# Performance work log

Hardware: AMD Instinct MI355X
Metric: run time of the kernel (lower is better)

Reference implementation:

```python
import jax, jax.numpy as jnp
import numpy as np

N_GRAPH = 100000
N_CAND = 1000
N_EDGES = 3200000
F_IN = 32


def _param(k, shape):
    return jax.random.normal(k, shape, dtype=jnp.float32) * 0.1


def setup_inputs() -> dict:
    key = jax.random.key(0)
    ks = jax.random.split(key, 20)
    inp = {
        "x": jax.random.normal(ks[0], (N_GRAPH, F_IN), dtype=jnp.float32),
        "candidate_set": jax.random.normal(ks[1], (N_CAND, F_IN), dtype=jnp.float32),
        "edge_index": jax.random.randint(ks[2], (2, N_EDGES), 0, N_GRAPH, dtype=jnp.int32),
        # GCN stack 32 -> 16 -> 24 -> 32
        "W1": _param(ks[3], (F_IN, 16)), "b1": jnp.zeros((16,), jnp.float32),
        "W2": _param(ks[4], (16, 24)),   "b2": jnp.zeros((24,), jnp.float32),
        "W3": _param(ks[5], (24, 32)),   "b3": jnp.zeros((32,), jnp.float32),
        # start-node MLP: 32 -> 16 -> 1
        "Ws1": _param(ks[6], (32, 16)), "bs1": jnp.zeros((16,), jnp.float32),
        "Ws2": _param(ks[7], (16, 1)),  "bs2": jnp.zeros((1,), jnp.float32),
        # end-node MLP: 32 -> 24 -> 1
        "We1": _param(ks[8], (32, 24)), "be1": jnp.zeros((24,), jnp.float32),
        "We2": _param(ks[9], (24, 1)),  "be2": jnp.zeros((1,), jnp.float32),
    }
    return inp


def _relu6(v):
    return jnp.clip(v, 0.0, 6.0)


def _gcn(h, row, col, dinv, W, b, N):
    # PyG GCNConv: h @ W, then D^-1/2 (A+I) D^-1/2 aggregation, then + bias
    h = h @ W
    norm = (dinv[row] * dinv[col])[:, None]
    return jax.ops.segment_sum(h[row] * norm, col, num_segments=N) + b


def reference(x, candidate_set, edge_index, W1, b1, W2, b2, W3, b3,
              Ws1, bs1, Ws2, bs2, We1, be1, We2, be2):
    n_graph = x.shape[0]
    h = jnp.concatenate([x, candidate_set], axis=0)  # [N, F_IN]
    N = h.shape[0]
    sl = jnp.arange(N, dtype=edge_index.dtype)
    row = jnp.concatenate([edge_index[0], sl])  # self-loops appended
    col = jnp.concatenate([edge_index[1], sl])
    deg = jax.ops.segment_sum(jnp.ones(row.shape[0], h.dtype), col, num_segments=N)
    dinv = 1.0 / jnp.sqrt(deg)  # deg >= 1 thanks to self-loops

    for W, b in ((W1, b1), (W2, b2), (W3, b3)):
        h = _gcn(h, row, col, dinv, W, b, N)  # [N, 32] at the end

    # start-node head: softmax over nodes (dim 0)
    start_probs = jax.nn.softmax(_relu6(h @ Ws1 + bs1) @ Ws2 + bs2, axis=0)  # [N,1]
    mask = jnp.ones_like(start_probs).at[n_graph:].set(0.0)  # zero out candidates
    start_probs = start_probs * mask
    start_probs = jnp.where(start_probs == 0.0, 1e-10, start_probs)
    start_probs = start_probs.squeeze()  # [N]
    start_node = jax.random.categorical(jax.random.key(42), jnp.log(start_probs))

    # end-node head
    end_probs = jax.nn.softmax(_relu6(h @ We1 + be1) @ We2 + be2, axis=0)  # [N,1]
    end_probs = end_probs.at[start_node].set(0.0)
    end_probs = jnp.where(end_probs == 0.0, 1e-10, end_probs)
    end_probs = end_probs.squeeze()  # [N]
    end_node = jax.random.categorical(jax.random.key(43), jnp.log(end_probs))

    new_edge = jnp.stack([start_node, end_node]).astype(edge_index.dtype)[:, None]
    edge_index_new = jnp.concatenate([edge_index, new_edge], axis=1)
    return (h, start_probs, end_probs, start_node, end_node, edge_index_new)
```

## Files before the change

kernel.cpp:

```cpp
#include <hip/hip_runtime.h>
#include <math.h>

#define TPB 256
#define BNODES 256
#define EPB 8192
#define SENT (-1)
#define MAXBKT 512
#define STAGE_CAP 14144

typedef _Float16 h8 __attribute__((ext_vector_type(8)));
typedef _Float16 hf;

__device__ __forceinline__ float jax_gumbel(unsigned key, unsigned i) {
  unsigned x0 = 0u, x1 = i;
  unsigned ks0 = 0u, ks1 = key, ks2 = key ^ 0x1BD11BDAu;
  x0 += ks0; x1 += ks1;
#define TFR(r) { x0 += x1; x1 = (x1 << (r)) | (x1 >> (32 - (r))); x1 ^= x0; }
  TFR(13) TFR(15) TFR(26) TFR(6)
  x0 += ks1; x1 += ks2 + 1u;
  TFR(17) TFR(29) TFR(16) TFR(24)
  x0 += ks2; x1 += ks0 + 2u;
  TFR(13) TFR(15) TFR(26) TFR(6)
  x0 += ks0; x1 += ks1 + 3u;
  TFR(17) TFR(29) TFR(16) TFR(24)
  x0 += ks1; x1 += ks2 + 4u;
  TFR(13) TFR(15) TFR(26) TFR(6)
  x0 += ks2; x1 += ks0 + 5u;
#undef TFR
  unsigned bits = x0 ^ x1;
  float f = __uint_as_float((bits >> 9) | 0x3f800000u) - 1.0f;
  float u = (f == 0.0f) ? 1.17549435e-38f : f;
  return -logf(-logf(u));
}

__global__ void hist_k(const int* __restrict__ col, int* __restrict__ hist,
                       int ne, int nbkt, int nblk) {
  __shared__ int h[1024];
  int t = threadIdx.x;
  for (int i = t; i < nbkt; i += TPB) h[i] = 0;
  __syncthreads();
  int base = blockIdx.x * EPB;
#pragma unroll
  for (int k = 0; k < EPB / TPB; k++) {
    int idx = base + k * TPB + t;
    if (idx < ne) atomicAdd(&h[col[idx] >> 8], 1);
  }
  __syncthreads();
  for (int i = t; i < nbkt; i += TPB) hist[(size_t)i * nblk + blockIdx.x] = h[i];
}

__global__ void breal_k(const int* __restrict__ hist, int* __restrict__ breal, int nblk) {
  int bkt = blockIdx.x;
  int t = threadIdx.x;
  int s = 0;
  for (int b = t; b < nblk; b += TPB) s += hist[(size_t)bkt * nblk + b];
  __shared__ int red[TPB];
  red[t] = s; __syncthreads();
  for (int st = 128; st > 0; st >>= 1) { if (t < st) red[t] += red[t + st]; __syncthreads(); }
  if (t == 0) breal[bkt] = red[0];
}

template <int PAD>
__global__ void scan1_k(const int* __restrict__ a, int* __restrict__ bsums, int n) {
  int t = threadIdx.x;
  int base = blockIdx.x * 1024 + t * 4;
  int s = 0;
#pragma unroll
  for (int k = 0; k < 4; k++) {
    int i = base + k;
    if (i < n) { int v = a[i]; if (PAD) v = (v + 15) & ~15; s += v; }
  }
  __shared__ int red[TPB];
  red[t] = s; __syncthreads();
  for (int st = 128; st > 0; st >>= 1) { if (t < st) red[t] += red[t + st]; __syncthreads(); }
  if (t == 0) bsums[blockIdx.x] = red[0];
}

__global__ void scan_single_k(int* a, int m) {
  __shared__ int sc[TPB];
  int t = threadIdx.x;
  int v[4]; int s = 0;
#pragma unroll
  for (int k = 0; k < 4; k++) { int i = t * 4 + k; v[k] = (i < m) ? a[i] : 0; s += v[k]; }
  sc[t] = s; __syncthreads();
  for (int off = 1; off < TPB; off <<= 1) {
    int add = (t >= off) ? sc[t - off] : 0;
    __syncthreads();
    sc[t] += add;
    __syncthreads();
  }
  int excl = sc[t] - s;
#pragma unroll
  for (int k = 0; k < 4; k++) { int i = t * 4 + k; if (i < m) a[i] = excl; excl += v[k]; }
  if (t == TPB - 1) a[m] = excl;
}

template <int PAD>
__global__ void scan3_k(const int* __restrict__ a, const int* __restrict__ bsums,
                        int* __restrict__ outp, int n, int nb) {
  int t = threadIdx.x;
  int base = blockIdx.x * 1024 + t * 4;
  int v[4]; int tsum = 0;
#pragma unroll
  for (int k = 0; k < 4; k++) {
    int vv = 0;
    if (base + k < n) { vv = a[base + k]; if (PAD) vv = (vv + 15) & ~15; }
    v[k] = vv; tsum += vv;
  }
  __shared__ int sc[TPB];
  sc[t] = tsum; __syncthreads();
  for (int off = 1; off < TPB; off <<= 1) {
    int add = (t >= off) ? sc[t - off] : 0;
    __syncthreads();
    sc[t] += add;
    __syncthreads();
  }
  int excl = sc[t] - tsum + bsums[blockIdx.x];
#pragma unroll
  for (int k = 0; k < 4; k++) { if (base + k < n) outp[base + k] = excl; excl += v[k]; }
  if (blockIdx.x == 0 && t == 0) outp[n] = bsums[nb];
}

__global__ void __launch_bounds__(TPB, 1)
bscatter_k(const int* __restrict__ row, const int* __restrict__ col,
           const int* __restrict__ histP, int* __restrict__ pairs,
           int ne, int nbkt, int nblk) {
  __shared__ int sbase[MAXBKT], lofs[MAXBKT], lcur[MAXBKT], lsz[MAXBKT];
  __shared__ int ssc[TPB];
  __shared__ int stage[STAGE_CAP];
  int t = threadIdx.x;
  int b = blockIdx.x;
  int i0 = 2 * t, i1 = 2 * t + 1;
  int g0 = 0, L0 = 0, g1 = 0, L1 = 0;
  if (i0 < nbkt) { size_t f = (size_t)i0 * nblk + b; g0 = histP[f]; L0 = histP[f + 1] - g0; }
  if (i1 < nbkt) { size_t f = (size_t)i1 * nblk + b; g1 = histP[f]; L1 = histP[f + 1] - g1; }
  int s = L0 + L1;
  ssc[t] = s; __syncthreads();
  for (int off = 1; off < TPB; off <<= 1) {
    int add = (t >= off) ? ssc[t - off] : 0;
    __syncthreads();
    ssc[t] += add;
    __syncthreads();
  }
  int excl = ssc[t] - s;
  if (i0 < nbkt) { sbase[i0] = g0; lofs[i0] = excl; lcur[i0] = excl; lsz[i0] = L0; }
  if (i1 < nbkt) { sbase[i1] = g1; lofs[i1] = excl + L0; lcur[i1] = excl + L0; lsz[i1] = L1; }
  __syncthreads();
  int base0 = b * EPB;
#pragma unroll
  for (int k = 0; k < EPB / TPB; k++) {
    int idx = base0 + k * TPB + t;
    if (idx < ne) {
      int c = col[idx];
      int r = row[idx];
      int p = atomicAdd(&lcur[c >> 8], 1);
      stage[p] = (r << 8) | (c & 255);
    }
  }
  __syncthreads();
  for (int i = t; i < nbkt; i += TPB) {
    int en = lcur[i], pe = lofs[i] + lsz[i];
    for (int p = en; p < pe; p++) stage[p] = SENT;
  }
  __syncthreads();
  int4* gp = (int4*)pairs;
  const int4* sp = (const int4*)stage;
  for (int i = t; i < nbkt; i += TPB) {
    int gb = sbase[i] >> 2, lb = lofs[i] >> 2, m = lsz[i] >> 2;
    for (int q = 0; q < m; q++) gp[gb + q] = sp[lb + q];
  }
}

__global__ void bbuild_k(const int* __restrict__ pairs, const int* __restrict__ histP,
                         const int* __restrict__ bbase, int nblk, int* __restrict__ rp,
                         float* __restrict__ dinv, int* __restrict__ csr, int n, int ne) {
  int bkt = blockIdx.x;
  int lo = bkt << 8;
  int t = threadIdx.x;
  int pstart = histP[(size_t)bkt * nblk];
  int pend   = histP[(size_t)(bkt + 1) * nblk];
  int rbase  = bbase[bkt];
  __shared__ int cnt[BNODES], sc[BNODES], pos[BNODES];
  cnt[t] = 0; __syncthreads();
  for (int p = pstart + t; p < pend; p += TPB) {
    int e = pairs[p];
    if (e >= 0) atomicAdd(&cnt[e & 255], 1);
  }
  __syncthreads();
  int own = cnt[t];
  sc[t] = own; __syncthreads();
  for (int off = 1; off < BNODES; off <<= 1) {
    int add = (t >= off) ? sc[t - off] : 0;
    __syncthreads();
    sc[t] += add;
    __syncthreads();
  }
  int excl = sc[t] - own;
  if (lo + t < n) {
    rp[lo + t] = rbase + excl;
    dinv[lo + t] = 1.0f / sqrtf((float)(own + 1));
  }
  pos[t] = rbase + excl;
  __syncthreads();
  for (int p = pstart + t; p < pend; p += TPB) {
    int e = pairs[p];
    if (e >= 0) {
      int q = atomicAdd(&pos[e & 255], 1);
      csr[q] = e >> 8;
    }
  }
  if (bkt == 0 && t == 0) rp[n] = ne;
}

__global__ void prep_k(const float* __restrict__ W2, const float* __restrict__ W3,
                       const float* __restrict__ b1, const float* __restrict__ b2,
                       float* __restrict__ W23, float* __restrict__ bvA, float* __restrict__ bvB) {
  int t = threadIdx.x;
  for (int idx = t; idx < 512; idx += TPB) {
    int i = idx >> 5, j = idx & 31;
    float s = 0.f;
    for (int k = 0; k < 24; k++) s += W2[i * 24 + k] * W3[k * 32 + j];
    W23[idx] = s;
  }
  __syncthreads();
  if (t < 32) {
    float sA = 0.f;
    for (int i = 0; i < 16; i++) sA += b1[i] * W23[i * 32 + t];
    bvA[t] = sA;
    float sB = 0.f;
    for (int k = 0; k < 24; k++) sB += b2[k] * W3[k * 32 + t];
    bvB[t] = sB;
  }
}

__global__ void gemm16h_k(const float* __restrict__ A, const float* __restrict__ A2, int nsplit,
                          const float* __restrict__ W, const float* __restrict__ dinv,
                          hf* __restrict__ out, int n) {
  constexpr int FIN = 32, FOUT = 16, FP = 16;
  constexpr int NODES = TPB / FP;
  __shared__ float Ws[FIN * FOUT];
  __shared__ float Hs[NODES * (FIN + 1)];
  int t = threadIdx.x;
  int base = blockIdx.x * NODES;
  for (int i = t; i < FIN * FOUT; i += TPB) Ws[i] = W[i];
  for (int i = t; i < NODES * FIN; i += TPB) {
    int nl = i / FIN, k = i - nl * FIN;
    int g = base + nl;
    float v = 0.f;
    if (g < n) v = (g < nsplit) ? A[(size_t)g * FIN + k] : A2[(size_t)(g - nsplit) * FIN + k];
    Hs[nl * (FIN + 1) + k] = v;
  }
  __syncthreads();
  int nl = t / FP, j = t % FP;
  int g = base + nl;
  if (g < n) {
    float acc = 0.f;
#pragma unroll
    for (int k = 0; k < FIN; k++) acc += Hs[nl * (FIN + 1) + k] * Ws[k * FOUT + j];
    out[(size_t)g * FOUT + j] = (hf)(acc * dinv[g]);
  }
}

__global__ void agghs_k(const h8* __restrict__ ts, const int* __restrict__ csr,
                        const int* __restrict__ rp, const float* __restrict__ dinv,
                        const float* __restrict__ sin, float* __restrict__ u_out,
                        float* __restrict__ us_out, h8* __restrict__ outv, int n) {
  int wave = blockIdx.x * (TPB / 64) + (threadIdx.x >> 6);
  int lane = threadIdx.x & 63;
  int j = lane & 1;
  int grp = (lane >> 1) & 7;
  int nl = lane >> 4;
  int c = wave * 4 + nl;
  bool valid = (c < n);
  float acc[8] = {0.f, 0.f, 0.f, 0.f, 0.f, 0.f, 0.f, 0.f};
  float accS = 0.f;
  if (valid) {
    int s = rp[c], e = rp[c + 1];
    for (int p = s + grp; p < e; p += 8) {
      int r = csr[p];
      h8 v = ts[r * 2 + j];
#pragma unroll
      for (int k = 0; k < 8; k++) acc[k] += (float)v[k];
      if (j == 0) accS += sin[r];
    }
  }
#pragma unroll
  for (int off = 2; off <= 8; off <<= 1) {
#pragma unroll
    for (int k = 0; k < 8; k++) acc[k] += __shfl_xor(acc[k], off, 64);
    accS += __shfl_xor(accS, off, 64);
  }
  if (valid && grp == 0) {
    h8 self = ts[c * 2 + j];
    float d = dinv[c];
    float scl = d * d;
    h8 o;
#pragma unroll
    for (int k = 0; k < 8; k++) o[k] = (hf)(scl * (acc[k] + (float)self[k]));
    outv[c * 2 + j] = o;
    if (j == 0) {
      float u = d * (accS + sin[c]);
      u_out[c] = u;
      if (us_out) us_out[c] = u * d;
    }
  }
}

__global__ void agghc_k(const h8* __restrict__ ts, const int* __restrict__ csr,
                        const int* __restrict__ rp, const float* __restrict__ dinv,
                        const float* __restrict__ a1, const float* __restrict__ a2,
                        const float* __restrict__ W23, const float* __restrict__ bvA,
                        const float* __restrict__ bvB, const float* __restrict__ b3,
                        float* __restrict__ out, int n) {
  __shared__ float Ws[512], vA[32], vB[32], vb[32];
  __shared__ float t3s[16][17];
  int t = threadIdx.x;
  for (int i = t; i < 512; i += TPB) Ws[i] = W23[i];
  if (t < 32) { vA[t] = bvA[t]; vB[t] = bvB[t]; vb[t] = b3[t]; }
  int wave = t >> 6;
  int lane = t & 63;
  int j = lane & 1;
  int grp = (lane >> 1) & 7;
  int nl = lane >> 4;
  int nlb = wave * 4 + nl;
  int c = blockIdx.x * 16 + nlb;
  bool valid = (c < n);
  float acc[8] = {0.f, 0.f, 0.f, 0.f, 0.f, 0.f, 0.f, 0.f};
  if (valid) {
    int s = rp[c], e = rp[c + 1];
    for (int p = s + grp; p < e; p += 8) {
      int r = csr[p];
      h8 v = ts[r * 2 + j];
#pragma unroll
      for (int k = 0; k < 8; k++) acc[k] += (float)v[k];
    }
  }
#pragma unroll
  for (int off = 2; off <= 8; off <<= 1) {
#pragma unroll
    for (int k = 0; k < 8; k++) acc[k] += __shfl_xor(acc[k], off, 64);
  }
  if (valid && grp == 0) {
    h8 self = ts[c * 2 + j];
    float d = dinv[c];
#pragma unroll
    for (int k = 0; k < 8; k++) t3s[nlb][j * 8 + k] = d * (acc[k] + (float)self[k]);
  }
  __syncthreads();
  int n2 = t >> 4, j2 = t & 15;
  int g = blockIdx.x * 16 + n2;
  if (g < n) {
    float accA = 0.f, accB = 0.f;
#pragma unroll
    for (int k = 0; k < 16; k++) {
      float h = t3s[n2][k];
      accA += h * Ws[k * 32 + j2];
      accB += h * Ws[k * 32 + j2 + 16];
    }
    float av = a1[g], bv = a2[g];
    out[(size_t)g * 32 + j2]      = accA + bv * vA[j2]      + av * vB[j2]      + vb[j2];
    out[(size_t)g * 32 + j2 + 16] = accB + bv * vA[j2 + 16] + av * vB[j2 + 16] + vb[j2 + 16];
  }
}

__global__ void heads_k(const float* __restrict__ h3,
                        const float* __restrict__ Ws1, const float* __restrict__ bs1,
                        const float* __restrict__ ws2, const float* __restrict__ bs2,
                        const float* __restrict__ We1, const float* __restrict__ be1,
                        const float* __restrict__ we2, const float* __restrict__ be2,
                        float* __restrict__ slog, float* __restrict__ elog, int n) {
  __shared__ float W1s[32 * 16], W2s[32 * 24], b1s[16], b2s[24], v1s[16], v2s[24];
  int t = threadIdx.x;
  for (int i = t; i < 32 * 16; i += TPB) W1s[i] = Ws1[i];
  for (int i = t; i < 32 * 24; i += TPB) W2s[i] = We1[i];
  if (t < 16) { b1s[t] = bs1[t]; v1s[t] = ws2[t]; }
  if (t < 24) { b2s[t] = be1[t]; v2s[t] = we2[t]; }
  __syncthreads();
  int i = blockIdx.x * TPB + t;
  if (i >= n) return;
  float row[32];
#pragma unroll
  for (int k = 0; k < 32; k++) row[k] = h3[(size_t)i * 32 + k];
  float s = bs2[0];
#pragma unroll
  for (int j = 0; j < 16; j++) {
    float a = b1s[j];
#pragma unroll
    for (int k = 0; k < 32; k++) a += row[k] * W1s[k * 16 + j];
    a = fminf(fmaxf(a, 0.f), 6.f);
    s += a * v1s[j];
  }
  float e2 = be2[0];
#pragma unroll
  for (int j = 0; j < 24; j++) {
    float a = b2s[j];
#pragma unroll
    for (int k = 0; k < 32; k++) a += row[k] * W2s[k * 24 + j];
    a = fminf(fmaxf(a, 0.f), 6.f);
    e2 += a * v2s[j];
  }
  slog[i] = s;
  elog[i] = e2;
}

__global__ void osm_k(const float* __restrict__ a, const float* __restrict__ b,
                      float* __restrict__ pm, int n) {
  int t = threadIdx.x;
  float m1 = -3.402823466e+38f, s1 = 0.f, m2 = -3.402823466e+38f, s2 = 0.f;
  for (int i = blockIdx.x * TPB + t; i < n; i += gridDim.x * TPB) {
    float x = a[i];
    if (x > m1) { s1 = s1 * expf(m1 - x) + 1.f; m1 = x; } else s1 += expf(x - m1);
    float y = b[i];
    if (y > m2) { s2 = s2 * expf(m2 - y) + 1.f; m2 = y; } else s2 += expf(y - m2);
  }
  __shared__ float sm1[TPB], ss1[TPB], sm2[TPB], ss2[TPB];
  sm1[t] = m1; ss1[t] = s1; sm2[t] = m2; ss2[t] = s2; __syncthreads();
  for (int st = 128; st > 0; st >>= 1) {
    if (t < st) {
      float M = fmaxf(sm1[t], sm1[t + st]);
      ss1[t] = ss1[t] * expf(sm1[t] - M) + ss1[t + st] * expf(sm1[t + st] - M);
      sm1[t] = M;
      float M2 = fmaxf(sm2[t], sm2[t + st]);
      ss2[t] = ss2[t] * expf(sm2[t] - M2) + ss2[t + st] * expf(sm2[t + st] - M2);
      sm2[t] = M2;
    }
    __syncthreads();
  }
  if (t == 0) {
    pm[blockIdx.x] = sm1[0]; pm[256 + blockIdx.x] = ss1[0];
    pm[512 + blockIdx.x] = sm2[0]; pm[768 + blockIdx.x] = ss2[0];
  }
}

__global__ void osm_fin_k(const float* __restrict__ pm, float* __restrict__ fsc, int nb) {
  int t = threadIdx.x;
  float m1 = (t < nb) ? pm[t] : -3.402823466e+38f;
  float s1 = (t < nb) ? pm[256 + t] : 0.f;
  float m2 = (t < nb) ? pm[512 + t] : -3.402823466e+38f;
  float s2 = (t < nb) ? pm[768 + t] : 0.f;
  __shared__ float sm1[TPB], ss1[TPB], sm2[TPB], ss2[TPB];
  sm1[t] = m1; ss1[t] = s1; sm2[t] = m2; ss2[t] = s2; __syncthreads();
  for (int st = 128; st > 0; st >>= 1) {
    if (t < st) {
      float M = fmaxf(sm1[t], sm1[t + st]);
      ss1[t] = ss1[t] * expf(sm1[t] - M) + ss1[t + st] * expf(sm1[t + st] - M);
      sm1[t] = M;
      float M2 = fmaxf(sm2[t], sm2[t + st]);
      ss2[t] = ss2[t] * expf(sm2[t] - M2) + ss2[t + st] * expf(sm2[t + st] - M2);
      sm2[t] = M2;
    }
    __syncthreads();
  }
  if (t == 0) { fsc[0] = sm1[0]; fsc[2] = ss1[0]; fsc[1] = sm2[0]; fsc[3] = ss2[0]; }
}

template <int HEAD>
__global__ void pargmax_k(const float* __restrict__ logit, const float* __restrict__ fsc,
                          const int* __restrict__ isc, float* __restrict__ outp,
                          unsigned key, int n, int ngraph, float* pval, int* pidx) {
  int t = threadIdx.x;
  float mx = fsc[HEAD], sm = fsc[2 + HEAD];
  int ban = HEAD ? isc[0] : -1;
  float bv = -3.402823466e+38f;
  int bi = 0x7fffffff;
  for (int i = blockIdx.x * TPB + t; i < n; i += gridDim.x * TPB) {
    float p = expf(logit[i] - mx) / sm;
    if (HEAD == 0) { if (i >= ngraph) p = 0.f; }
    else           { if (i == ban) p = 0.f; }
    if (p == 0.f) p = 1e-10f;
    outp[i] = p;
    float v = logf(p) + jax_gumbel(key, (unsigned)i);
    if (v > bv) { bv = v; bi = i; }
  }
  __shared__ float sv[TPB]; __shared__ int si[TPB];
  sv[t] = bv; si[t] = bi; __syncthreads();
  for (int st = 128; st > 0; st >>= 1) {
    if (t < st) {
      float v2 = sv[t + st]; int i2 = si[t + st];
      if (v2 > sv[t] || (v2 == sv[t] && i2 < si[t])) { sv[t] = v2; si[t] = i2; }
    }
    __syncthreads();
  }
  if (t == 0) { pval[blockIdx.x] = sv[0]; pidx[blockIdx.x] = si[0]; }
}

__global__ void argmax_fin_k(const float* pval, const int* pidx, int nb,
                             int* isc, float* dnode) {
  int t = threadIdx.x;
  float bv = (t < nb) ? pval[t] : -3.402823466e+38f;
  int bi = (t < nb) ? pidx[t] : 0x7fffffff;
  __shared__ float sv[TPB]; __shared__ int si[TPB];
  sv[t] = bv; si[t] = bi; __syncthreads();
  for (int st = 128; st > 0; st >>= 1) {
    if (t < st) {
      float v2 = sv[t + st]; int i2 = si[t + st];
      if (v2 > sv[t] || (v2 == sv[t] && i2 < si[t])) { sv[t] = v2; si[t] = i2; }
    }
    __syncthreads();
  }
  if (t == 0) { isc[0] = si[0]; dnode[0] = (float)si[0]; }
}

__global__ void argmax_fin_end_k(const float* pval, const int* pidx, int nb,
                                 const int* isc, float* p_end, float* p_e0, float* p_e1) {
  int t = threadIdx.x;
  float bv = (t < nb) ? pval[t] : -3.402823466e+38f;
  int bi = (t < nb) ? pidx[t] : 0x7fffffff;
  __shared__ float sv[TPB]; __shared__ int si[TPB];
  sv[t] = bv; si[t] = bi; __syncthreads();
  for (int st = 128; st > 0; st >>= 1) {
    if (t < st) {
      float v2 = sv[t + st]; int i2 = si[t + st];
      if (v2 > sv[t] || (v2 == sv[t] && i2 < si[t])) { sv[t] = v2; si[t] = i2; }
    }
    __syncthreads();
  }
  if (t == 0) {
    int en = si[0];
    p_end[0] = (float)en;
    p_e0[0] = (float)isc[0];
    p_e1[0] = (float)en;
  }
}

__global__ void edgecopy4_k(const int4* __restrict__ ei4, float* __restrict__ outp, int ne) {
  int i = blockIdx.x * TPB + threadIdx.x;
  int ne4 = ne / 4;
  if (i < ne4) {
    int4 r = ei4[i];
    float4 f = make_float4((float)r.x, (float)r.y, (float)r.z, (float)r.w);
    ((float4*)outp)[i] = f;
    int4 c = ei4[ne4 + i];
    float* o1 = outp + (size_t)(ne + 1) + i * 4;
    o1[0] = (float)c.x; o1[1] = (float)c.y; o1[2] = (float)c.z; o1[3] = (float)c.w;
  }
}

__global__ void edgecopy_sc_k(const int* __restrict__ ei, float* __restrict__ outp, int ne) {
  int i = blockIdx.x * TPB + threadIdx.x;
  if (i < 2 * ne) {
    int r = (i >= ne);
    int e = i - r * ne;
    outp[(size_t)r * (ne + 1) + e] = (float)ei[i];
  }
}

extern "C" void kernel_launch(void* const* d_in, const int* in_sizes, int n_in,
                              void* d_out, int out_size, void* d_ws, size_t ws_size,
                              hipStream_t stream) {
  const float* x    = (const float*)d_in[0];
  const float* cand = (const float*)d_in[1];
  const int*   ei   = (const int*)d_in[2];
  const float* W1 = (const float*)d_in[3];  const float* b1  = (const float*)d_in[4];
  const float* W2 = (const float*)d_in[5];  const float* b2  = (const float*)d_in[6];
  const float* W3 = (const float*)d_in[7];  const float* b3  = (const float*)d_in[8];
  const float* Ws1= (const float*)d_in[9];  const float* bs1 = (const float*)d_in[10];
  const float* Ws2= (const float*)d_in[11]; const float* bs2 = (const float*)d_in[12];
  const float* We1= (const float*)d_in[13]; const float* be1 = (const float*)d_in[14];
  const float* We2= (const float*)d_in[15]; const float* be2 = (const float*)d_in[16];

  const int nG = in_sizes[0] / 32, nC = in_sizes[1] / 32;
  const int n  = nG + nC;
  const int ne = in_sizes[2] / 2;

  float* out = (float*)d_out;
  const size_t OFF1 = (size_t)n * 32;
  const size_t OFF2 = OFF1 + n;
  const size_t OFF3 = OFF2 + n;
  const size_t OFF4 = OFF3 + 1;
  const size_t OFF5 = OFF4 + 1;

  float* wf = (float*)d_ws;
  int*   wi = (int*)d_ws;
  size_t NP = (((size_t)n + 2) + 63) & ~(size_t)63;
  size_t o = 0;
  int*   rp    = wi + o; o += NP;
  int*   bsums = wi + o; o += 384;
  int*   breal = wi + o; o += 512;
  float* dinv  = wf + o; o += NP;
  float* a1v   = wf + o; o += NP;
  float* a1s   = wf + o; o += NP;
  float* a2v   = wf + o; o += NP;
  float* w23   = wf + o; o += 512;
  float* bvA   = wf + o; o += 64;
  float* bvB   = wf + o; o += 64;
  float* bufX  = wf + o; o += (size_t)n * 32 + 64;
  float* bufT  = wf + o; o += (size_t)n * 32 + 64;
  float* slogv = wf + o; o += NP;
  float* elogv = wf + o; o += NP;
  float* pmA   = wf + o; o += 1024;
  float* aval  = wf + o; o += 512;
  int*   aidx  = wi + o; o += 512;
  float* fsc   = wf + o; o += 64;
  int*   isc   = wi + o; o += 64;

  int* pairs = (int*)bufX;
  hf*  hh0   = (hf*)bufT;
  hf*  hh1   = hh0 + (size_t)n * 16;
  int*  csr  = (int*)(out + OFF5);
  int*  hist = csr + ne;

  const int* row = ei;
  const int* col = ei + ne;

  const int NBKT = (n + BNODES - 1) / BNODES;
  const int NBLK = (ne + EPB - 1) / EPB;
  const int H    = NBKT * NBLK;
  const int nbh  = (H + 1023) / 1024;

  int gN = (n + TPB - 1) / TPB;
  int ne4 = ne / 4;

  hist_k<<<NBLK, TPB, 0, stream>>>(col, hist, ne, NBKT, NBLK);
  breal_k<<<NBKT, TPB, 0, stream>>>(hist, breal, NBLK);
  scan_single_k<<<1, TPB, 0, stream>>>(breal, NBKT);
  scan1_k<1><<<nbh, TPB, 0, stream>>>(hist, bsums, H);
  scan_single_k<<<1, TPB, 0, stream>>>(bsums, nbh);
  scan3_k<1><<<nbh, TPB, 0, stream>>>(hist, bsums, hist, H, nbh);
  bscatter_k<<<NBLK, TPB, 0, stream>>>(row, col, hist, pairs, ne, NBKT, NBLK);
  bbuild_k<<<NBKT, TPB, 0, stream>>>(pairs, hist, breal, NBLK, rp, dinv, csr, n, ne);

  prep_k<<<1, TPB, 0, stream>>>(W2, W3, b1, b2, w23, bvA, bvB);
  gemm16h_k<<<(n + 15) / 16, TPB, 0, stream>>>(x, cand, nG, W1, dinv, hh0, n);
  agghs_k<<<(n + 15) / 16, TPB, 0, stream>>>((const h8*)hh0, csr, rp, dinv, dinv, a1v, a1s,
                                             (h8*)hh1, n);
  agghs_k<<<(n + 15) / 16, TPB, 0, stream>>>((const h8*)hh1, csr, rp, dinv, a1s, a2v, nullptr,
                                             (h8*)hh0, n);
  agghc_k<<<(n + 15) / 16, TPB, 0, stream>>>((const h8*)hh0, csr, rp, dinv, a1v, a2v,
                                             w23, bvA, bvB, b3, out, n);

  if (ne % 4 == 0) {
    edgecopy4_k<<<(ne4 + TPB - 1) / TPB, TPB, 0, stream>>>((const int4*)ei, out + OFF5, ne);
  } else {
    edgecopy_sc_k<<<(2 * ne + TPB - 1) / TPB, TPB, 0, stream>>>(ei, out + OFF5, ne);
  }

  heads_k<<<gN, TPB, 0, stream>>>(out, Ws1, bs1, Ws2, bs2, We1, be1, We2, be2, slogv, elogv, n);
  osm_k<<<256, TPB, 0, stream>>>(slogv, elogv, pmA, n);
  osm_fin_k<<<1, TPB, 0, stream>>>(pmA, fsc, 256);

  pargmax_k<0><<<256, TPB, 0, stream>>>(slogv, fsc, nullptr, out + OFF1, 42u, n, nG, aval, aidx);
  argmax_fin_k<<<1, TPB, 0, stream>>>(aval, aidx, 256, isc, out + OFF3);

  pargmax_k<1><<<256, TPB, 0, stream>>>(elogv, fsc, isc, out + OFF2, 43u, n, nG, aval + 256, aidx + 256);
  argmax_fin_end_k<<<1, TPB, 0, stream>>>(aval + 256, aidx + 256, 256, isc,
                                          out + OFF4, out + OFF5 + ne, out + OFF5 + 2 * (size_t)ne + 1);
}
```

Measured before the change: 367.6 us.

## Fuse edge copy into scatter, softmax stats into heads, narrow aggregation groups

The edge-index float conversion now happens inside the bucket scatter kernel, which removes a separate copy kernel. The online-softmax partial reduction is folded into the heads kernel, and the final reducer loops over the larger number of block partials. The aggregation kernels now use 4 lanes per node instead of 8, so each wave handles 8 nodes. This suits the low average degree and cuts the shuffle reduction steps. Workspace buffers (csr, hist, pairs) move from the output region into dedicated workspace, and pmA grows to hold up to 512 partials per statistic, which gN (about 395) fits.

```diff
diff --git a/kernel.cpp b/kernel.cpp
--- a/kernel.cpp
+++ b/kernel.cpp
@@ -124,6 +124,7 @@
 __global__ void __launch_bounds__(TPB, 1)
 bscatter_k(const int* __restrict__ row, const int* __restrict__ col,
            const int* __restrict__ histP, int* __restrict__ pairs,
+           float* __restrict__ e0, float* __restrict__ e1,
            int ne, int nbkt, int nblk) {
   __shared__ int sbase[MAXBKT], lofs[MAXBKT], lcur[MAXBKT], lsz[MAXBKT];
   __shared__ int ssc[TPB];
@@ -155,6 +156,8 @@
       int r = row[idx];
       int p = atomicAdd(&lcur[c >> 8], 1);
       stage[p] = (r << 8) | (c & 255);
+      e0[idx] = (float)r;
+      e1[idx] = (float)c;
     }
   }
   __syncthreads();
@@ -268,15 +271,15 @@
   int wave = blockIdx.x * (TPB / 64) + (threadIdx.x >> 6);
   int lane = threadIdx.x & 63;
   int j = lane & 1;
-  int grp = (lane >> 1) & 7;
-  int nl = lane >> 4;
-  int c = wave * 4 + nl;
+  int grp = (lane >> 1) & 3;
+  int nl = lane >> 3;
+  int c = wave * 8 + nl;
   bool valid = (c < n);
   float acc[8] = {0.f, 0.f, 0.f, 0.f, 0.f, 0.f, 0.f, 0.f};
   float accS = 0.f;
   if (valid) {
     int s = rp[c], e = rp[c + 1];
-    for (int p = s + grp; p < e; p += 8) {
+    for (int p = s + grp; p < e; p += 4) {
       int r = csr[p];
       h8 v = ts[r * 2 + j];
 #pragma unroll
@@ -285,7 +288,7 @@
     }
   }
 #pragma unroll
-  for (int off = 2; off <= 8; off <<= 1) {
+  for (int off = 2; off <= 4; off <<= 1) {
 #pragma unroll
     for (int k = 0; k < 8; k++) acc[k] += __shfl_xor(acc[k], off, 64);
     accS += __shfl_xor(accS, off, 64);
@@ -313,22 +316,22 @@
                         const float* __restrict__ bvB, const float* __restrict__ b3,
                         float* __restrict__ out, int n) {
   __shared__ float Ws[512], vA[32], vB[32], vb[32];
-  __shared__ float t3s[16][17];
+  __shared__ float t3s[32][17];
   int t = threadIdx.x;
   for (int i = t; i < 512; i += TPB) Ws[i] = W23[i];
   if (t < 32) { vA[t] = bvA[t]; vB[t] = bvB[t]; vb[t] = b3[t]; }
   int wave = t >> 6;
   int lane = t & 63;
   int j = lane & 1;
-  int grp = (lane >> 1) & 7;
-  int nl = lane >> 4;
-  int nlb = wave * 4 + nl;
-  int c = blockIdx.x * 16 + nlb;
+  int grp = (lane >> 1) & 3;
+  int nl = lane >> 3;
+  int nlb = wave * 8 + nl;
+  int c = blockIdx.x * 32 + nlb;
   bool valid = (c < n);
   float acc[8] = {0.f, 0.f, 0.f, 0.f, 0.f, 0.f, 0.f, 0.f};
   if (valid) {
     int s = rp[c], e = rp[c + 1];
-    for (int p = s + grp; p < e; p += 8) {
+    for (int p = s + grp; p < e; p += 4) {
       int r = csr[p];
       h8 v = ts[r * 2 + j];
 #pragma unroll
@@ -336,7 +339,7 @@
     }
   }
 #pragma unroll
-  for (int off = 2; off <= 8; off <<= 1) {
+  for (int off = 2; off <= 4; off <<= 1) {
 #pragma unroll
     for (int k = 0; k < 8; k++) acc[k] += __shfl_xor(acc[k], off, 64);
   }
@@ -347,19 +350,18 @@
     for (int k = 0; k < 8; k++) t3s[nlb][j * 8 + k] = d * (acc[k] + (float)self[k]);
   }
   __syncthreads();
-  int n2 = t >> 4, j2 = t & 15;
-  int g = blockIdx.x * 16 + n2;
+  int n2 = t >> 3, jb = t & 7;
+  int g = blockIdx.x * 32 + n2;
   if (g < n) {
-    float accA = 0.f, accB = 0.f;
-#pragma unroll
-    for (int k = 0; k < 16; k++) {
-      float h = t3s[n2][k];
-      accA += h * Ws[k * 32 + j2];
-      accB += h * Ws[k * 32 + j2 + 16];
-    }
     float av = a1[g], bv = a2[g];
-    out[(size_t)g * 32 + j2]      = accA + bv * vA[j2]      + av * vB[j2]      + vb[j2];
-    out[(size_t)g * 32 + j2 + 16] = accB + bv * vA[j2 + 16] + av * vB[j2 + 16] + vb[j2 + 16];
+#pragma unroll
+    for (int q = 0; q < 4; q++) {
+      int j2 = jb + q * 8;
+      float acc2 = 0.f;
+#pragma unroll
+      for (int k = 0; k < 16; k++) acc2 += t3s[n2][k] * Ws[k * 32 + j2];
+      out[(size_t)g * 32 + j2] = acc2 + bv * vA[j2] + av * vB[j2] + vb[j2];
+    }
   }
 }
 
@@ -368,7 +370,8 @@
                         const float* __restrict__ ws2, const float* __restrict__ bs2,
                         const float* __restrict__ We1, const float* __restrict__ be1,
                         const float* __restrict__ we2, const float* __restrict__ be2,
-                        float* __restrict__ slog, float* __restrict__ elog, int n) {
+                        float* __restrict__ slog, float* __restrict__ elog,
+                        float* __restrict__ pm, int n) {
   __shared__ float W1s[32 * 16], W2s[32 * 24], b1s[16], b2s[24], v1s[16], v2s[24];
   int t = threadIdx.x;
   for (int i = t; i < 32 * 16; i += TPB) W1s[i] = Ws1[i];
@@ -377,44 +380,36 @@
   if (t < 24) { b2s[t] = be1[t]; v2s[t] = we2[t]; }
   __syncthreads();
   int i = blockIdx.x * TPB + t;
-  if (i >= n) return;
-  float row[32];
-#pragma unroll
-  for (int k = 0; k < 32; k++) row[k] = h3[(size_t)i * 32 + k];
-  float s = bs2[0];
-#pragma unroll
-  for (int j = 0; j < 16; j++) {
-    float a = b1s[j];
-#pragma unroll
-    for (int k = 0; k < 32; k++) a += row[k] * W1s[k * 16 + j];
-    a = fminf(fmaxf(a, 0.f), 6.f);
-    s += a * v1s[j];
-  }
-  float e2 = be2[0];
-#pragma unroll
-  for (int j = 0; j < 24; j++) {
-    float a = b2s[j];
-#pragma unroll
-    for (int k = 0; k < 32; k++) a += row[k] * W2s[k * 24 + j];
-    a = fminf(fmaxf(a, 0.f), 6.f);
-    e2 += a * v2s[j];
-  }
-  slog[i] = s;
-  elog[i] = e2;
-}
-
-__global__ void osm_k(const float* __restrict__ a, const float* __restrict__ b,
-                      float* __restrict__ pm, int n) {
-  int t = threadIdx.x;
-  float m1 = -3.402823466e+38f, s1 = 0.f, m2 = -3.402823466e+38f, s2 = 0.f;
-  for (int i = blockIdx.x * TPB + t; i < n; i += gridDim.x * TPB) {
-    float x = a[i];
-    if (x > m1) { s1 = s1 * expf(m1 - x) + 1.f; m1 = x; } else s1 += expf(x - m1);
-    float y = b[i];
-    if (y > m2) { s2 = s2 * expf(m2 - y) + 1.f; m2 = y; } else s2 += expf(y - m2);
+  float s = -3.402823466e+38f, e2 = -3.402823466e+38f;
+  if (i < n) {
+    float row[32];
+#pragma unroll
+    for (int k = 0; k < 32; k++) row[k] = h3[(size_t)i * 32 + k];
+    s = bs2[0];
+#pragma unroll
+    for (int j = 0; j < 16; j++) {
+      float a = b1s[j];
+#pragma unroll
+      for (int k = 0; k < 32; k++) a += row[k] * W1s[k * 16 + j];
+      a = fminf(fmaxf(a, 0.f), 6.f);
+      s += a * v1s[j];
+    }
+    e2 = be2[0];
+#pragma unroll
+    for (int j = 0; j < 24; j++) {
+      float a = b2s[j];
+#pragma unroll
+      for (int k = 0; k < 32; k++) a += row[k] * W2s[k * 24 + j];
+      a = fminf(fmaxf(a, 0.f), 6.f);
+      e2 += a * v2s[j];
+    }
+    slog[i] = s;
+    elog[i] = e2;
   }
   __shared__ float sm1[TPB], ss1[TPB], sm2[TPB], ss2[TPB];
-  sm1[t] = m1; ss1[t] = s1; sm2[t] = m2; ss2[t] = s2; __syncthreads();
+  sm1[t] = s;  ss1[t] = (i < n) ? 1.f : 0.f;
+  sm2[t] = e2; ss2[t] = (i < n) ? 1.f : 0.f;
+  __syncthreads();
   for (int st = 128; st > 0; st >>= 1) {
     if (t < st) {
       float M = fmaxf(sm1[t], sm1[t + st]);
@@ -427,17 +422,22 @@
     __syncthreads();
   }
   if (t == 0) {
-    pm[blockIdx.x] = sm1[0]; pm[256 + blockIdx.x] = ss1[0];
-    pm[512 + blockIdx.x] = sm2[0]; pm[768 + blockIdx.x] = ss2[0];
+    pm[blockIdx.x] = sm1[0]; pm[512 + blockIdx.x] = ss1[0];
+    pm[1024 + blockIdx.x] = sm2[0]; pm[1536 + blockIdx.x] = ss2[0];
   }
 }
 
 __global__ void osm_fin_k(const float* __restrict__ pm, float* __restrict__ fsc, int nb) {
   int t = threadIdx.x;
-  float m1 = (t < nb) ? pm[t] : -3.402823466e+38f;
-  float s1 = (t < nb) ? pm[256 + t] : 0.f;
-  float m2 = (t < nb) ? pm[512 + t] : -3.402823466e+38f;
-  float s2 = (t < nb) ? pm[768 + t] : 0.f;
+  float m1 = -3.402823466e+38f, s1 = 0.f, m2 = -3.402823466e+38f, s2 = 0.f;
+  for (int i = t; i < nb; i += TPB) {
+    float bm1 = pm[i], bs1v = pm[512 + i];
+    float M = fmaxf(m1, bm1);
+    s1 = s1 * expf(m1 - M) + bs1v * expf(bm1 - M); m1 = M;
+    float bm2 = pm[1024 + i], bs2v = pm[1536 + i];
+    float M2 = fmaxf(m2, bm2);
+    s2 = s2 * expf(m2 - M2) + bs2v * expf(bm2 - M2); m2 = M2;
+  }
   __shared__ float sm1[TPB], ss1[TPB], sm2[TPB], ss2[TPB];
   sm1[t] = m1; ss1[t] = s1; sm2[t] = m2; ss2[t] = s2; __syncthreads();
   for (int st = 128; st > 0; st >>= 1) {
@@ -520,28 +520,6 @@
     p_end[0] = (float)en;
     p_e0[0] = (float)isc[0];
     p_e1[0] = (float)en;
-  }
-}
-
-__global__ void edgecopy4_k(const int4* __restrict__ ei4, float* __restrict__ outp, int ne) {
-  int i = blockIdx.x * TPB + threadIdx.x;
-  int ne4 = ne / 4;
-  if (i < ne4) {
-    int4 r = ei4[i];
-    float4 f = make_float4((float)r.x, (float)r.y, (float)r.z, (float)r.w);
-    ((float4*)outp)[i] = f;
-    int4 c = ei4[ne4 + i];
-    float* o1 = outp + (size_t)(ne + 1) + i * 4;
-    o1[0] = (float)c.x; o1[1] = (float)c.y; o1[2] = (float)c.z; o1[3] = (float)c.w;
-  }
-}
-
-__global__ void edgecopy_sc_k(const int* __restrict__ ei, float* __restrict__ outp, int ne) {
-  int i = blockIdx.x * TPB + threadIdx.x;
-  if (i < 2 * ne) {
-    int r = (i >= ne);
-    int e = i - r * ne;
-    outp[(size_t)r * (ne + 1) + e] = (float)ei[i];
   }
 }
 
@@ -569,6 +547,11 @@
   const size_t OFF3 = OFF2 + n;
   const size_t OFF4 = OFF3 + 1;
   const size_t OFF5 = OFF4 + 1;
+
+  const int NBKT = (n + BNODES - 1) / BNODES;
+  const int NBLK = (ne + EPB - 1) / EPB;
+  const int H    = NBKT * NBLK;
+  const int nbh  = (H + 1023) / 1024;
 
   float* wf = (float*)d_ws;
   int*   wi = (int*)d_ws;
@@ -584,32 +567,23 @@
   float* w23   = wf + o; o += 512;
   float* bvA   = wf + o; o += 64;
   float* bvB   = wf + o; o += 64;
-  float* bufX  = wf + o; o += (size_t)n * 32 + 64;
-  float* bufT  = wf + o; o += (size_t)n * 32 + 64;
   float* slogv = wf + o; o += NP;
   float* elogv = wf + o; o += NP;
-  float* pmA   = wf + o; o += 1024;
+  float* pmA   = wf + o; o += 2048;
   float* aval  = wf + o; o += 512;
   int*   aidx  = wi + o; o += 512;
   float* fsc   = wf + o; o += 64;
   int*   isc   = wi + o; o += 64;
-
-  int* pairs = (int*)bufX;
-  hf*  hh0   = (hf*)bufT;
-  hf*  hh1   = hh0 + (size_t)n * 16;
-  int*  csr  = (int*)(out + OFF5);
-  int*  hist = csr + ne;
+  hf*    hh0   = (hf*)(wf + o); o += (size_t)n * 8 + 64;
+  hf*    hh1   = (hf*)(wf + o); o += (size_t)n * 8 + 64;
+  int*   hist  = wi + o; o += (size_t)H + 64;
+  int*   csr   = wi + o; o += (size_t)ne + 64;
+  int*   pairs = wi + o; o += (size_t)ne + 15 * (size_t)H + 64;
 
   const int* row = ei;
   const int* col = ei + ne;
 
-  const int NBKT = (n + BNODES - 1) / BNODES;
-  const int NBLK = (ne + EPB - 1) / EPB;
-  const int H    = NBKT * NBLK;
-  const int nbh  = (H + 1023) / 1024;
-
   int gN = (n + TPB - 1) / TPB;
-  int ne4 = ne / 4;
 
   hist_k<<<NBLK, TPB, 0, stream>>>(col, hist, ne, NBKT, NBLK);
   breal_k<<<NBKT, TPB, 0, stream>>>(hist, breal, NBLK);
@@ -617,27 +591,21 @@
   scan1_k<1><<<nbh, TPB, 0, stream>>>(hist, bsums, H);
   scan_single_k<<<1, TPB, 0, stream>>>(bsums, nbh);
   scan3_k<1><<<nbh, TPB, 0, stream>>>(hist, bsums, hist, H, nbh);
-  bscatter_k<<<NBLK, TPB, 0, stream>>>(row, col, hist, pairs, ne, NBKT, NBLK);
+  bscatter_k<<<NBLK, TPB, 0, stream>>>(row, col, hist, pairs,
+                                       out + OFF5, out + OFF5 + ne + 1, ne, NBKT, NBLK);
   bbuild_k<<<NBKT, TPB, 0, stream>>>(pairs, hist, breal, NBLK, rp, dinv, csr, n, ne);
 
   prep_k<<<1, TPB, 0, stream>>>(W2, W3, b1, b2, w23, bvA, bvB);
   gemm16h_k<<<(n + 15) / 16, TPB, 0, stream>>>(x, cand, nG, W1, dinv, hh0, n);
-  agghs_k<<<(n + 15) / 16, TPB, 0, stream>>>((const h8*)hh0, csr, rp, dinv, dinv, a1v, a1s,
-                                             (h8*)hh1, n);
-  agghs_k<<<(n + 15) / 16, TPB, 0, stream>>>((const h8*)hh1, csr, rp, dinv, a1s, a2v, nullptr,
-                                             (h8*)hh0, n);
-  agghc_k<<<(n + 15) / 16, TPB, 0, stream>>>((const h8*)hh0, csr, rp, dinv, a1v, a2v,
-                                             w23, bvA, bvB, b3, out, n);
-
-  if (ne % 4 == 0) {
-    edgecopy4_k<<<(ne4 + TPB - 1) / TPB, TPB, 0, stream>>>((const int4*)ei, out + OFF5, ne);
-  } else {
-    edgecopy_sc_k<<<(2 * ne + TPB - 1) / TPB, TPB, 0, stream>>>(ei, out + OFF5, ne);
-  }
-
-  heads_k<<<gN, TPB, 0, stream>>>(out, Ws1, bs1, Ws2, bs2, We1, be1, We2, be2, slogv, elogv, n);
-  osm_k<<<256, TPB, 0, stream>>>(slogv, elogv, pmA, n);
-  osm_fin_k<<<1, TPB, 0, stream>>>(pmA, fsc, 256);
+  int gH = (n + 31) / 32;
+  agghs_k<<<gH, TPB, 0, stream>>>((const h8*)hh0, csr, rp, dinv, dinv, a1v, a1s, (h8*)hh1, n);
+  agghs_k<<<gH, TPB, 0, stream>>>((const h8*)hh1, csr, rp, dinv, a1s, a2v, nullptr, (h8*)hh0, n);
+  agghc_k<<<gH, TPB, 0, stream>>>((const h8*)hh0, csr, rp, dinv, a1v, a2v,
+                                  w23, bvA, bvB, b3, out, n);
+
+  heads_k<<<gN, TPB, 0, stream>>>(out, Ws1, bs1, Ws2, bs2, We1, be1, We2, be2,
+                                  slogv, elogv, pmA, n);
+  osm_fin_k<<<1, TPB, 0, stream>>>(pmA, fsc, gN);
 
   pargmax_k<0><<<256, TPB, 0, stream>>>(slogv, fsc, nullptr, out + OFF1, 42u, n, nG, aval, aidx);
   argmax_fin_k<<<1, TPB, 0, stream>>>(aval, aidx, 256, isc, out + OFF3);
```

New measurement: 470.9 us. +28.1%, slower.
